# Kernel optimization log

Hardware: AMD Instinct MI355X
Metric: run time of the kernel (lower is better)

Reference implementation:

```python
import jax, jax.numpy as jnp
import numpy as np

DIM = 32
NUM_BLOCKS = 6
XP_DIM = 16
TP_DIM = 8


def _init_lin(key, fan_in, fan_out):
    kw, kb = jax.random.split(key)
    s = 1.0 / np.sqrt(fan_in)
    W = jax.random.uniform(kw, (fan_in, fan_out), jnp.float32, -s, s)
    b = jax.random.uniform(kb, (fan_out,), jnp.float32, -s, s)
    return W, b


def setup_inputs() -> dict:
    key = jax.random.key(0)
    ks = jax.random.split(key, 24)
    B, N = 16, 256
    inp = {
        'coords': jax.random.normal(ks[0], (B, N, 2), jnp.float32),
        'x_params': jax.random.normal(ks[1], (B, 8, 2), jnp.float32),
        't_params': jax.random.normal(ks[2], (B, TP_DIM), jnp.float32),
    }
    # xp2ex: DNN([16,32,32],'sin')
    inp['xp2ex_W1'], inp['xp2ex_b1'] = _init_lin(ks[3], XP_DIM, DIM)
    inp['xp2ex_W2'], inp['xp2ex_b2'] = _init_lin(ks[4], DIM, DIM)
    # tp2et: DNN([8,32,32],'sin')
    inp['tp2et_W1'], inp['tp2et_b1'] = _init_lin(ks[5], TP_DIM, DIM)
    inp['tp2et_W2'], inp['tp2et_b2'] = _init_lin(ks[6], DIM, DIM)
    # initial hidden states (learnable; random instead of zeros for testing)
    inp['h0'] = 0.1 * jax.random.normal(ks[7], (1, DIM), jnp.float32)
    inp['gh0'] = 0.1 * jax.random.normal(ks[8], (1, DIM), jnp.float32)
    fWh, fbh, fWz, fbz = [], [], [], []
    for i in range(NUM_BLOCKS):
        W, b = _init_lin(ks[9 + i], DIM, DIM); fWh.append(W); fbh.append(b)
        W, b = _init_lin(jax.random.fold_in(ks[9 + i], 1), 2 + DIM, DIM); fWz.append(W); fbz.append(b)
    inp['f_Wh'], inp['f_bh'] = jnp.stack(fWh), jnp.stack(fbh)
    inp['f_Wz'], inp['f_bz'] = jnp.stack(fWz), jnp.stack(fbz)
    gWh, gbh, gWz, gbz = [], [], [], []
    for i in range(NUM_BLOCKS):
        W, b = _init_lin(ks[15 + i], DIM, DIM); gWh.append(W); gbh.append(b)
        W, b = _init_lin(jax.random.fold_in(ks[15 + i], 1), DIM + DIM, DIM); gWz.append(W); gbz.append(b)
    inp['g_Wh'], inp['g_bh'] = jnp.stack(gWh), jnp.stack(gbh)
    inp['g_Wz'], inp['g_bz'] = jnp.stack(gWz), jnp.stack(gbz)
    # d: SymmetricInitDNN([32,1],'identity') -> single linear
    inp['d_W'], inp['d_b'] = _init_lin(ks[21], DIM, 1)
    return inp


def reference(coords, x_params, t_params,
              xp2ex_W1, xp2ex_b1, xp2ex_W2, xp2ex_b2,
              tp2et_W1, tp2et_b1, tp2et_W2, tp2et_b2,
              h0, gh0,
              f_Wh, f_bh, f_Wz, f_bz,
              g_Wh, g_bh, g_Wz, g_bz,
              d_W, d_b):
    B, N = coords.shape[0], coords.shape[1]
    x = coords[..., 0:1]   # (B, N, 1)
    t = coords[..., 1:2]   # (B, N, 1)
    # conditioning embeddings (2-layer sin MLPs, linear output)
    xp = x_params.reshape(B, -1)                                   # (B, 16)
    ex = jnp.sin(xp @ xp2ex_W1 + xp2ex_b1) @ xp2ex_W2 + xp2ex_b2   # (B, 32)
    et = jnp.sin(t_params @ tp2et_W1 + tp2et_b1) @ tp2et_W2 + tp2et_b2  # (B, 32)
    # broadcast to (B, Nt, Nx, .) grid
    tr = jnp.broadcast_to(t[:, :, None, :], (B, N, N, 1))
    xr = jnp.broadcast_to(x[:, None, :, :], (B, N, N, 1))
    etu = jnp.broadcast_to(et[:, None, None, :], (B, N, N, DIM))
    ztpx = jnp.concatenate([xr, tr, etu], axis=-1)  # (B, N, N, 34)

    def block_step(h, w):
        Wh, bh, Wz, bz = w
        return jnp.sin(h @ Wh + bh + h_cond @ Wz + bz), None

    # f-stream: modulated-SIREN blocks conditioned on (x, t, et)
    h_cond = ztpx
    h = jnp.broadcast_to(h0[None, None], (B, N, N, DIM))
    h, _ = jax.lax.scan(block_step, h, (f_Wh, f_bh, f_Wz, f_bz))
    # g-stream: conditioned on (h, ex)
    ex_b = jnp.broadcast_to(ex[:, None, None, :], (B, N, N, DIM))
    h_cond = jnp.concatenate([h, ex_b], axis=-1)  # (B, N, N, 64)
    gh = jnp.broadcast_to(gh0[None, None], (B, N, N, DIM))
    gh, _ = jax.lax.scan(block_step, gh, (g_Wh, g_bh, g_Wz, g_bz))
    u_pred = gh @ d_W + d_b  # (B, N, N, 1)
    return u_pred
```

## Files before the change

kernel.cpp:

```cpp
#include <hip/hip_runtime.h>

#define DIM 32
#define NB  6
#define INV2PI 0.15915494309189535f

typedef __attribute__((ext_vector_type(8)))  _Float16 half8;
typedef __attribute__((ext_vector_type(16))) float floatx16;

union H8I4 { half8 h; int i[4]; };

__device__ __forceinline__ int pkrne(float a, float b) {
    _Float16 h0 = (_Float16)a, h1 = (_Float16)b;
    unsigned short u0, u1;
    __builtin_memcpy(&u0, &h0, 2); __builtin_memcpy(&u1, &h1, 2);
    return (int)(u0 | ((unsigned)u1 << 16));
}
#if __has_builtin(__builtin_amdgcn_cvt_pkrtz)
__device__ __forceinline__ int pkrtz(float a, float b) {
    auto h = __builtin_amdgcn_cvt_pkrtz(a, b);
    int r; __builtin_memcpy(&r, &h, 4); return r;
}
#else
#define pkrtz pkrne
#endif

__device__ __forceinline__ int Pmap(int s, int h, int j) { return 16*s + 8*(j>>2) + 4*h + (j&3); }
__device__ __forceinline__ int Qmap(int p)               { int r = p & 15, h = p >> 4; return 8*(r>>2) + 4*h + (r&3); }

#define MFMA(a, b, c) __builtin_amdgcn_mfma_f32_32x32x16_f16((a), (b), (c), 0, 0, 0)

__device__ __forceinline__ void sinsplit(const floatx16& acc, half8& b1, half8& b2) {
    H8I4 n1, n2;
    #pragma unroll
    for (int q = 0; q < 4; ++q) {
        n1.i[q] = pkrtz(__builtin_amdgcn_sinf(acc[2*q]),
                        __builtin_amdgcn_sinf(acc[2*q+1]));
        n2.i[q] = pkrtz(__builtin_amdgcn_sinf(acc[8+2*q]),
                        __builtin_amdgcn_sinf(acc[8+2*q+1]));
    }
    b1 = n1.h; b2 = n2.h;
}

#define LDS_BYTES 36480

__global__ __launch_bounds__(512, 4) void sep_mfma(
    const float* __restrict__ coords,
    const float* __restrict__ x_params,
    const float* __restrict__ t_params,
    const float* __restrict__ xW1, const float* __restrict__ xb1,
    const float* __restrict__ xW2, const float* __restrict__ xb2,
    const float* __restrict__ tW1, const float* __restrict__ tb1,
    const float* __restrict__ tW2, const float* __restrict__ tb2,
    const float* __restrict__ h0,  const float* __restrict__ gh0,
    const float* __restrict__ f_Wh, const float* __restrict__ f_bh,
    const float* __restrict__ f_Wz, const float* __restrict__ f_bz,
    const float* __restrict__ g_Wh, const float* __restrict__ g_bh,
    const float* __restrict__ g_Wz, const float* __restrict__ g_bz,
    const float* __restrict__ d_W,  const float* __restrict__ d_b,
    float* __restrict__ out)
{
    extern __shared__ char smem[];
    float* sfz0p  = (float*)smem;
    float* sfz1p  = sfz0p + 192;
    float* sCgp   = sfz1p + 192;
    float* rawCfP = sCgp + 192;
    float* sdWp   = rawCfP + 192;
    float* shx    = sdWp + 32;
    float* sht    = shx + 32;
    float* sex    = sht + 32;
    float* set_   = sex + 32;
    unsigned short* sImg = (unsigned short*)(set_ + 32);

    const int tid = threadIdx.x;
    const int b   = blockIdx.x >> 6;
    const int ig  = (blockIdx.x >> 1) & 31;
    const int jg  = blockIdx.x & 1;

    if (tid < 32) {
        float a = xb1[tid];
        for (int k = 0; k < 16; ++k) a = fmaf(x_params[b * 16 + k], xW1[k * 32 + tid], a);
        shx[tid] = __sinf(a);
    } else if (tid < 64) {
        int d = tid - 32;
        float a = tb1[d];
        for (int k = 0; k < 8; ++k) a = fmaf(t_params[b * 8 + k], tW1[k * 32 + d], a);
        sht[d] = __sinf(a);
    }
    {
        int* sImgI = (int*)sImg;
        for (int ii = tid; ii < 8192; ii += 512) {
            int region = ii >> 9;
            int r = ii & 511;
            int s = r >> 8, t = r & 255;
            int lane = t >> 2, jj2 = t & 3;
            int m = lane & 31, hg = lane >> 5;
            int c0 = 16*s + 8*(jj2 >> 1) + 4*hg + 2*(jj2 & 1);
            float w0, w1;
            if (region < 5)       { int l = region + 1;  w0 = f_Wh[(l*32 + c0)*32 + m]; w1 = f_Wh[(l*32 + c0 + 1)*32 + m]; }
            else if (region < 10) { int l = region - 4;  w0 = g_Wh[(l*32 + c0)*32 + m]; w1 = g_Wh[(l*32 + c0 + 1)*32 + m]; }
            else                  { int l = region - 10; w0 = g_Wz[(l*64 + c0)*32 + m]; w1 = g_Wz[(l*64 + c0 + 1)*32 + m]; }
            sImgI[ii] = pkrne(w0 * INV2PI, w1 * INV2PI);
        }
    }
    __syncthreads();

    if (tid < 32) {
        float a = xb2[tid];
        for (int c = 0; c < 32; ++c) a = fmaf(shx[c], xW2[c * 32 + tid], a);
        sex[tid] = a;
    } else if (tid < 64) {
        int d = tid - 32;
        float a = tb2[d];
        for (int c = 0; c < 32; ++c) a = fmaf(sht[c], tW2[c * 32 + d], a);
        set_[d] = a;
    }
    if (tid < 192) {
        int l = tid >> 5, p = tid & 31, d = Qmap(p);
        sfz0p[tid] = f_Wz[(l * 34 + 0) * 32 + d] * INV2PI;
        sfz1p[tid] = f_Wz[(l * 34 + 1) * 32 + d] * INV2PI;
    }
    if (tid < 32) sdWp[tid] = d_W[Qmap(tid)];
    __syncthreads();

    if (tid < 192) {
        int l = tid >> 5, p = tid & 31, d = Qmap(p);
        float a = f_bh[l * 32 + d] + f_bz[l * 32 + d];
        for (int c = 0; c < 32; ++c) a = fmaf(set_[c], f_Wz[(l * 34 + 2 + c) * 32 + d], a);
        if (l == 0)
            for (int c = 0; c < 32; ++c) a = fmaf(h0[c], f_Wh[c * 32 + d], a);
        rawCfP[tid] = a * INV2PI;
        float g = g_bh[l * 32 + d] + g_bz[l * 32 + d];
        for (int c = 0; c < 32; ++c) g = fmaf(sex[c], g_Wz[(l * 64 + 32 + c) * 32 + d], g);
        if (l == 0)
            for (int c = 0; c < 32; ++c) g = fmaf(gh0[c], g_Wh[c * 32 + d], g);
        sCgp[tid] = g * INV2PI;
    }
    __syncthreads();

    const int lane = tid & 63, wave = tid >> 6;
    const int i = ig * 8 + wave;
    const int e = lane & 31, hk = lane >> 5;
    const int pb = hk * 16;
    const float ti = coords[(b * 256 + i) * 2 + 1];
    const float db = d_b[0];

    #pragma unroll 1
    for (int t = 0; t < 4; ++t) {
        const int tile = jg * 4 + t;
        const int j = tile * 32 + e;
        const float xj = coords[(b * 256 + j) * 2];

        floatx16 acc;
        half8 hB1, hB2;

        {
            const float* cf = &rawCfP[pb];
            const float* z0 = &sfz0p[pb];
            const float* z1 = &sfz1p[pb];
            #pragma unroll
            for (int r = 0; r < 16; ++r) acc[r] = fmaf(xj, z0[r], fmaf(ti, z1[r], cf[r]));
            sinsplit(acc, hB1, hB2);
        }
        for (int l = 1; l < NB; ++l) {
            const float* cf = &rawCfP[l * 32 + pb];
            const float* z0 = &sfz0p[l * 32 + pb];
            const float* z1 = &sfz1p[l * 32 + pb];
            #pragma unroll
            for (int r = 0; r < 16; ++r) acc[r] = fmaf(xj, z0[r], fmaf(ti, z1[r], cf[r]));
            const unsigned short* base = &sImg[((l - 1) * 2) * 512 + lane * 8];
            half8 ah0 = *(const half8*)(base);
            half8 ah1 = *(const half8*)(base + 512);
            acc = MFMA(ah0, hB1, acc);
            acc = MFMA(ah1, hB2, acc);
            sinsplit(acc, hB1, hB2);
        }

        half8 gB1, gB2;
        {
            const float* cg = &sCgp[pb];
            #pragma unroll
            for (int r = 0; r < 16; ++r) acc[r] = cg[r];
            const unsigned short* bz = &sImg[10240 + lane * 8];
            half8 wz0 = *(const half8*)(bz);
            half8 wz1 = *(const half8*)(bz + 512);
            acc = MFMA(wz0, hB1, acc);
            acc = MFMA(wz1, hB2, acc);
            sinsplit(acc, gB1, gB2);
        }
        for (int l = 1; l < NB; ++l) {
            const float* cg = &sCgp[l * 32 + pb];
            #pragma unroll
            for (int r = 0; r < 16; ++r) acc[r] = cg[r];
            {
                const unsigned short* bh = &sImg[5120 + ((l - 1) * 2) * 512 + lane * 8];
                half8 wh0 = *(const half8*)(bh);
                half8 wh1 = *(const half8*)(bh + 512);
                acc = MFMA(wh0, gB1, acc);
                acc = MFMA(wh1, gB2, acc);
            }
            __builtin_amdgcn_sched_barrier(0);
            {
                const unsigned short* bz = &sImg[10240 + (l * 2) * 512 + lane * 8];
                half8 wz0 = *(const half8*)(bz);
                half8 wz1 = *(const half8*)(bz + 512);
                acc = MFMA(wz0, hB1, acc);
                acc = MFMA(wz1, hB2, acc);
            }
            if (l < NB - 1) sinsplit(acc, gB1, gB2);
        }

        float u = 0.0f;
        #pragma unroll
        for (int r = 0; r < 16; ++r) u = fmaf(__builtin_amdgcn_sinf(acc[r]), sdWp[pb + r], u);
        u += __shfl_xor(u, 32);
        if (hk == 0) out[(b * 256 + i) * 256 + j] = u + db;
    }
}

extern "C" void kernel_launch(void* const* d_in, const int* in_sizes, int n_in,
                              void* d_out, int out_size, void* d_ws, size_t ws_size,
                              hipStream_t stream) {
    const float* coords   = (const float*)d_in[0];
    const float* x_params = (const float*)d_in[1];
    const float* t_params = (const float*)d_in[2];
    const float* xW1 = (const float*)d_in[3];
    const float* xb1 = (const float*)d_in[4];
    const float* xW2 = (const float*)d_in[5];
    const float* xb2 = (const float*)d_in[6];
    const float* tW1 = (const float*)d_in[7];
    const float* tb1 = (const float*)d_in[8];
    const float* tW2 = (const float*)d_in[9];
    const float* tb2 = (const float*)d_in[10];
    const float* h0  = (const float*)d_in[11];
    const float* gh0 = (const float*)d_in[12];
    const float* f_Wh = (const float*)d_in[13];
    const float* f_bh = (const float*)d_in[14];
    const float* f_Wz = (const float*)d_in[15];
    const float* f_bz = (const float*)d_in[16];
    const float* g_Wh = (const float*)d_in[17];
    const float* g_bh = (const float*)d_in[18];
    const float* g_Wz = (const float*)d_in[19];
    const float* g_bz = (const float*)d_in[20];
    const float* d_W  = (const float*)d_in[21];
    const float* d_b  = (const float*)d_in[22];

    hipFuncSetAttribute((const void*)sep_mfma,
                        hipFuncAttributeMaxDynamicSharedMemorySize, LDS_BYTES);

    sep_mfma<<<1024, 512, LDS_BYTES, stream>>>(
        coords, x_params, t_params, xW1, xb1, xW2, xb2, tW1, tb1, tW2, tb2,
        h0, gh0, f_Wh, f_bh, f_Wz, f_bz, g_Wh, g_bh, g_Wz, g_bz, d_W, d_b,
        (float*)d_out);
}
```

Measured before the change: 167.6 us.

## Inject coordinate terms via split-fp16 MFMA instead of per-element FMAs

Measured after the change: 158.1 us. 1.06x faster.

```diff
diff --git a/kernel.cpp b/kernel.cpp
--- a/kernel.cpp
+++ b/kernel.cpp
@@ -41,7 +41,7 @@
     b1 = n1.h; b2 = n2.h;
 }
 
-#define LDS_BYTES 36480
+#define LDS_BYTES 38528
 
 __global__ __launch_bounds__(512, 4) void sep_mfma(
     const float* __restrict__ coords,
@@ -60,16 +60,16 @@
     float* __restrict__ out)
 {
     extern __shared__ char smem[];
-    float* sfz0p  = (float*)smem;
-    float* sfz1p  = sfz0p + 192;
-    float* sCgp   = sfz1p + 192;
+    float* sCgp   = (float*)smem;
     float* rawCfP = sCgp + 192;
     float* sdWp   = rawCfP + 192;
     float* shx    = sdWp + 32;
     float* sht    = shx + 32;
     float* sex    = sht + 32;
     float* set_   = sex + 32;
-    unsigned short* sImg = (unsigned short*)(set_ + 32);
+    unsigned short* sImg  = (unsigned short*)(set_ + 32);
+    unsigned short* sInj  = sImg + 16384;
+    unsigned short* sZero = sInj + 1536;
 
     const int tid = threadIdx.x;
     const int b   = blockIdx.x >> 6;
@@ -86,6 +86,7 @@
         for (int k = 0; k < 8; ++k) a = fmaf(t_params[b * 8 + k], tW1[k * 32 + d], a);
         sht[d] = __sinf(a);
     }
+    if (tid < 128) ((int*)sZero)[tid] = 0;
     {
         int* sImgI = (int*)sImg;
         for (int ii = tid; ii < 8192; ii += 512) {
@@ -115,9 +116,16 @@
         set_[d] = a;
     }
     if (tid < 192) {
-        int l = tid >> 5, p = tid & 31, d = Qmap(p);
-        sfz0p[tid] = f_Wz[(l * 34 + 0) * 32 + d] * INV2PI;
-        sfz1p[tid] = f_Wz[(l * 34 + 1) * 32 + d] * INV2PI;
+        int l = tid >> 5, m = tid & 31;
+        float z0 = f_Wz[(l * 34 + 0) * 32 + m] * INV2PI;
+        float z1 = f_Wz[(l * 34 + 1) * 32 + m] * INV2PI;
+        _Float16 h0_ = (_Float16)z0; float z0h = (float)h0_, z0l = z0 - z0h;
+        _Float16 h1_ = (_Float16)z1; float z1h = (float)h1_, z1l = z1 - z1h;
+        int* p = (int*)sInj + 4 * tid;
+        p[0] = pkrne(z0h, z0h);
+        p[1] = pkrne(z0l, z1h);
+        p[2] = pkrne(z1h, z1l);
+        p[3] = 0;
     }
     if (tid < 32) sdWp[tid] = d_W[Qmap(tid)];
     __syncthreads();
@@ -144,29 +152,46 @@
     const float ti = coords[(b * 256 + i) * 2 + 1];
     const float db = d_b[0];
 
+    float th_, tl_;
+    { _Float16 h = (_Float16)ti; th_ = (float)h; tl_ = ti - th_; }
+
+    const unsigned short* injbase = hk ? sZero : (sInj + e * 8);
+    const int injstep = hk ? 0 : 256;
+
     #pragma unroll 1
     for (int t = 0; t < 4; ++t) {
         const int tile = jg * 4 + t;
         const int j = tile * 32 + e;
         const float xj = coords[(b * 256 + j) * 2];
 
+        float xh_, xl_;
+        { _Float16 h = (_Float16)xj; xh_ = (float)h; xl_ = xj - xh_; }
+        H8I4 xtb;
+        xtb.i[0] = pkrtz(xh_, xl_);
+        xtb.i[1] = pkrtz(xh_, th_);
+        xtb.i[2] = pkrtz(tl_, th_);
+        xtb.i[3] = 0;
+        const half8 xtB = xtb.h;
+
         floatx16 acc;
         half8 hB1, hB2;
+        const unsigned short* ip = injbase;
 
         {
             const float* cf = &rawCfP[pb];
-            const float* z0 = &sfz0p[pb];
-            const float* z1 = &sfz1p[pb];
-            #pragma unroll
-            for (int r = 0; r < 16; ++r) acc[r] = fmaf(xj, z0[r], fmaf(ti, z1[r], cf[r]));
+            #pragma unroll
+            for (int r = 0; r < 16; ++r) acc[r] = cf[r];
+            half8 ia = *(const half8*)ip; ip += injstep;
+            acc = MFMA(ia, xtB, acc);
             sinsplit(acc, hB1, hB2);
         }
         for (int l = 1; l < NB; ++l) {
+            __builtin_amdgcn_sched_barrier(0);
             const float* cf = &rawCfP[l * 32 + pb];
-            const float* z0 = &sfz0p[l * 32 + pb];
-            const float* z1 = &sfz1p[l * 32 + pb];
-            #pragma unroll
-            for (int r = 0; r < 16; ++r) acc[r] = fmaf(xj, z0[r], fmaf(ti, z1[r], cf[r]));
+            #pragma unroll
+            for (int r = 0; r < 16; ++r) acc[r] = cf[r];
+            half8 ia = *(const half8*)ip; ip += injstep;
+            acc = MFMA(ia, xtB, acc);
             const unsigned short* base = &sImg[((l - 1) * 2) * 512 + lane * 8];
             half8 ah0 = *(const half8*)(base);
             half8 ah1 = *(const half8*)(base + 512);
```
